# Optimization experiments

Hardware: AMD Instinct MI355X
Metric: run time of the kernel (lower is better)

The kernel has to match this reference:

```python
import jax, jax.numpy as jnp
import numpy as np

HEADS = 8

def _grid_edges(H, W):
    # 4-neighbor grid adjacency, built at trace time (static), faithful to the torch double loop
    N = H * W
    idx = np.arange(N).reshape(H, W)
    e = np.zeros((N, N), np.float32)
    a, b = idx[1:, :].ravel(), idx[:-1, :].ravel()
    e[a, b] = 1.0; e[b, a] = 1.0
    a, b = idx[:, 1:].ravel(), idx[:, :-1].ravel()
    e[a, b] = 1.0; e[b, a] = 1.0
    return jnp.asarray(e)

def _layernorm(x, g, b, eps=1e-5):
    m = x.mean(-1, keepdims=True)
    v = x.var(-1, keepdims=True)
    return (x - m) / jnp.sqrt(v + eps) * g + b

def _gat(nodes, edges, W, b, rel):
    # nodes: [N,B,E]; W: [4,E,E] (q,k,v,out); rel: [HEADS]
    N, B, E = nodes.shape
    hd = E // HEADS
    q = (nodes @ W[0].T + b[0]).reshape(N, B, HEADS, hd)
    k = (nodes @ W[1].T + b[1]).reshape(N, B, HEADS, hd)
    v = (nodes @ W[2].T + b[2]).reshape(N, B, HEADS, hd)
    s = jnp.einsum('ibhd,jbhd->hbij', q, k) / float(np.sqrt(hd))
    s = s + edges[None, None] * rel[:, None, None, None]  # per-head edge relation bias
    a = jax.nn.softmax(s, axis=1)  # faithful to source: softmax over dim=1 (batch axis)
    o = jnp.einsum('hbij,jbhd->ibhd', a, v).reshape(N, B, E)
    return o @ W[3].T + b[3]

def _mha(q_in, kv_in, W, b):
    # standard nn.MultiheadAttention (eval, no dropout); seq-first [L,B,E]
    L, B, E = q_in.shape
    S = kv_in.shape[0]
    hd = E // HEADS
    q = (q_in @ W[0].T + b[0]).reshape(L, B, HEADS, hd)
    k = (kv_in @ W[1].T + b[1]).reshape(S, B, HEADS, hd)
    v = (kv_in @ W[2].T + b[2]).reshape(S, B, HEADS, hd)
    s = jnp.einsum('ibhd,jbhd->hbij', q, k) / float(np.sqrt(hd))
    a = jax.nn.softmax(s, axis=-1)
    o = jnp.einsum('hbij,jbhd->ibhd', a, v).reshape(L, B, E)
    return o @ W[3].T + b[3]

def reference(x, gat_W, gat_b, gat_rel, cross_W, cross_b, ln_g, ln_b):
    B, C, H, W = x.shape
    P = H // 4
    # global nodes: avg_pool2d(kernel=4) then flatten to [P*P, B, C]
    g = x.reshape(B, C, P, 4, P, 4).mean(axis=(3, 5))
    global_nodes = g.reshape(B, C, P * P).transpose(2, 0, 1)
    global_edges = jnp.ones((P * P, P * P), x.dtype)
    local_nodes = x.reshape(B, C, H * W).transpose(2, 0, 1)  # [HW,B,C]
    local_edges = _grid_edges(H, W)
    g_out = _gat(global_nodes, global_edges, gat_W[0], gat_b[0], gat_rel[0])
    g_out = _layernorm(g_out + global_nodes, ln_g[0], ln_b[0])
    l_out = _gat(local_nodes, local_edges, gat_W[1], gat_b[1], gat_rel[1])
    l_out = _layernorm(l_out + local_nodes, ln_g[1], ln_b[1])
    # nearest upsample x4 of global output back to HxW
    g_map = g_out.transpose(1, 2, 0).reshape(B, C, P, P)
    g_up = jnp.repeat(jnp.repeat(g_map, 4, axis=2), 4, axis=3)
    g_up = g_up.reshape(B, C, H * W).transpose(2, 0, 1)
    c_out = _mha(l_out, g_up, cross_W, cross_b)
    c_out = _layernorm(c_out + l_out, ln_g[2], ln_b[2])
    return c_out.transpose(1, 2, 0).reshape(B, C, H, W)

def setup_inputs() -> dict:
    key = jax.random.key(0)
    ks = jax.random.split(key, 6)
    B, C, H, W = 2, 256, 40, 40
    E = C
    sc = 0.02
    return {
        "x": jax.random.normal(ks[0], (B, C, H, W), jnp.float32),
        "gat_W": jax.random.normal(ks[1], (2, 4, E, E), jnp.float32) * sc,
        "gat_b": jax.random.normal(ks[2], (2, 4, E), jnp.float32) * sc,
        "gat_rel": jax.random.normal(ks[3], (2, HEADS), jnp.float32),
        "cross_W": jax.random.normal(ks[4], (4, E, E), jnp.float32) * sc,
        "cross_b": jax.random.normal(ks[5], (4, E), jnp.float32) * sc,
        "ln_g": jnp.ones((3, E), jnp.float32),
        "ln_b": jnp.zeros((3, E), jnp.float32),
    }
```

## Files before the change

### kernel.cpp

```cpp
#include <hip/hip_runtime.h>
#include <math.h>

#define NLOC 1600
#define NGLO 100

typedef unsigned short u16;
typedef short s16x8 __attribute__((ext_vector_type(8)));
typedef float f32x4 __attribute__((ext_vector_type(4)));

__device__ __forceinline__ short f2bf(float f) {
    unsigned u = __float_as_uint(f);
    u += 0x7fffu + ((u >> 16) & 1u);
    return (short)(u >> 16);
}
__device__ __forceinline__ float bf2f(u16 h) {
    return __uint_as_float(((unsigned)h) << 16);
}

__device__ __forceinline__ void gemm_core(int lane, const u16* __restrict__ A,
                                          const u16* __restrict__ W,
                                          int M, int m0, int n0, f32x4 acc[2][4]) {
    int c = lane & 15, qd = lane >> 4;
#pragma unroll
    for (int mi = 0; mi < 2; ++mi)
#pragma unroll
        for (int ni = 0; ni < 4; ++ni) acc[mi][ni] = (f32x4){0.f, 0.f, 0.f, 0.f};
#pragma unroll 2
    for (int kc = 0; kc < 8; ++kc) {
        int ko = kc * 32 + qd * 8;
        s16x8 af[2], bf[4];
#pragma unroll
        for (int mi = 0; mi < 2; ++mi) {
            int row = m0 + mi * 16 + c;
            s16x8 zz = {};
            af[mi] = (row < M) ? *(const s16x8*)(A + (size_t)row * 256 + ko) : zz;
        }
#pragma unroll
        for (int ni = 0; ni < 4; ++ni)
            bf[ni] = *(const s16x8*)(W + (size_t)(n0 + ni * 16 + c) * 256 + ko);
#pragma unroll
        for (int mi = 0; mi < 2; ++mi)
#pragma unroll
            for (int ni = 0; ni < 4; ++ni)
                acc[mi][ni] = __builtin_amdgcn_mfma_f32_16x16x32_bf16(af[mi], bf[ni],
                                                                      acc[mi][ni], 0, 0, 0);
    }
}

__device__ __forceinline__ void ep_row(int lane, f32x4 acc[2][4],
                                       const float* __restrict__ bias,
                                       u16* __restrict__ C, int M, int m0, int n0) {
    int c = lane & 15, qd = lane >> 4;
#pragma unroll
    for (int mi = 0; mi < 2; ++mi)
#pragma unroll
        for (int r = 0; r < 4; ++r) {
            int row = m0 + mi * 16 + 4 * qd + r;
            if (row < M) {
#pragma unroll
                for (int ni = 0; ni < 4; ++ni) {
                    int col = n0 + ni * 16 + c;
                    C[(size_t)row * 256 + col] = (u16)f2bf(acc[mi][ni][r] + bias[col]);
                }
            }
        }
}

__device__ __forceinline__ void ep_vt(int lane, f32x4 acc[2][4],
                                      const float* __restrict__ bias,
                                      u16* __restrict__ vt, int Npad,
                                      int M, int m0, int n0, float* sum) {
    int c = lane & 15, qd = lane >> 4;
    float s[4] = {0.f, 0.f, 0.f, 0.f};
#pragma unroll
    for (int mi = 0; mi < 2; ++mi)
#pragma unroll
        for (int r = 0; r < 4; ++r) {
            int row = m0 + mi * 16 + 4 * qd + r;
            if (row < M) {
                int n = row >> 1, b = row & 1;
#pragma unroll
                for (int ni = 0; ni < 4; ++ni) {
                    int col = n0 + ni * 16 + c;
                    float val = acc[mi][ni][r] + bias[col];
                    vt[(size_t)(b * 256 + col) * Npad + n] = (u16)f2bf(val);
                    if (b) s[ni] += val;
                }
            }
        }
    if (sum) {
#pragma unroll
        for (int ni = 0; ni < 4; ++ni)
            atomicAdd(&sum[n0 + ni * 16 + c], s[ni]);
    }
}

__device__ __forceinline__ void ep_vt_staged(int lane, u16* vtile,
                                             f32x4 acc[2][4],
                                             const float* __restrict__ bias,
                                             u16* __restrict__ vt, int Npad,
                                             int M, int m0, int n0, float* sum) {
    int c = lane & 15, qd = lane >> 4;
    float s[4] = {0.f, 0.f, 0.f, 0.f};
#pragma unroll
    for (int mi = 0; mi < 2; ++mi)
#pragma unroll
        for (int r = 0; r < 4; ++r) {
            int row = m0 + mi * 16 + 4 * qd + r;
            int b = r & 1;
            int n_loc = mi * 8 + 2 * qd + (r >> 1);
            bool ok = (row < M);
#pragma unroll
            for (int ni = 0; ni < 4; ++ni) {
                int col = n0 + ni * 16 + c;
                float val = ok ? (acc[mi][ni][r] + bias[col]) : 0.f;
                vtile[(b * 64 + ni * 16 + c) * 16 + n_loc] = (u16)f2bf(val);
                if (b && ok) s[ni] += val;
            }
        }
    asm volatile("s_waitcnt lgkmcnt(0)" ::: "memory");
    int nst = m0 >> 1;
#pragma unroll
    for (int b2 = 0; b2 < 2; ++b2) {
        const u16* src = vtile + (b2 * 64 + lane) * 16;
        s16x8 v0 = *(const s16x8*)src;
        s16x8 v1 = *(const s16x8*)(src + 8);
        u16* dst = vt + (size_t)(b2 * 256 + n0 + lane) * Npad + nst;
        *(s16x8*)dst = v0;
        *(s16x8*)(dst + 8) = v1;
    }
    if (sum) {
#pragma unroll
        for (int ni = 0; ni < 4; ++ni)
            atomicAdd(&sum[n0 + ni * 16 + c], s[ni]);
    }
}

template <int MODE>
__device__ __forceinline__ void gemmln_block(int tid, const u16* __restrict__ A,
                                             const u16* __restrict__ W,
                                             const float* __restrict__ bias,
                                             const float* __restrict__ R,
                                             const float* __restrict__ g,
                                             const float* __restrict__ bb,
                                             float* fout, u16* bfout, float* dout,
                                             int M, int m0) {
    int w = tid >> 6, lane = tid & 63;
    int c = lane & 15, qd = lane >> 4;
    int n0 = w * 64;

    f32x4 acc[4] = {};
#pragma unroll 2
    for (int kc = 0; kc < 8; ++kc) {
        int ko = kc * 32 + qd * 8;
        int row = m0 + c;
        s16x8 zz = {};
        s16x8 af = (row < M) ? *(const s16x8*)(A + (size_t)row * 256 + ko) : zz;
#pragma unroll
        for (int ni = 0; ni < 4; ++ni) {
            s16x8 bf = *(const s16x8*)(W + (size_t)(n0 + ni * 16 + c) * 256 + ko);
            acc[ni] = __builtin_amdgcn_mfma_f32_16x16x32_bf16(af, bf, acc[ni], 0, 0, 0);
        }
    }

    __shared__ float ps1[4][16], ps2[4][16];
    float v[4][4];
#pragma unroll
    for (int r = 0; r < 4; ++r) {
        int row = m0 + 4 * qd + r;
        bool ok = (row < M);
        float s1 = 0.f, s2 = 0.f;
#pragma unroll
        for (int ni = 0; ni < 4; ++ni) {
            int col = n0 + ni * 16 + c;
            float val = acc[ni][r] + bias[col] + (ok ? R[(size_t)row * 256 + col] : 0.f);
            v[r][ni] = val;
            s1 += val; s2 += val * val;
        }
        s1 += __shfl_xor(s1, 1); s2 += __shfl_xor(s2, 1);
        s1 += __shfl_xor(s1, 2); s2 += __shfl_xor(s2, 2);
        s1 += __shfl_xor(s1, 4); s2 += __shfl_xor(s2, 4);
        s1 += __shfl_xor(s1, 8); s2 += __shfl_xor(s2, 8);
        if (c == 0) { ps1[w][4 * qd + r] = s1; ps2[w][4 * qd + r] = s2; }
    }
    __syncthreads();

    if (MODE == 0) {
#pragma unroll
        for (int r = 0; r < 4; ++r) {
            int lr = 4 * qd + r;
            int row = m0 + lr;
            if (row >= M) continue;
            float s1 = ps1[0][lr] + ps1[1][lr] + ps1[2][lr] + ps1[3][lr];
            float s2 = ps2[0][lr] + ps2[1][lr] + ps2[2][lr] + ps2[3][lr];
            float mean = s1 * (1.f / 256.f);
            float var  = s2 * (1.f / 256.f) - mean * mean;
            float rstd = rsqrtf(var + 1e-5f);
#pragma unroll
            for (int ni = 0; ni < 4; ++ni) {
                int col = n0 + ni * 16 + c;
                float y = (v[r][ni] - mean) * rstd * g[col] + bb[col];
                fout[(size_t)row * 256 + col] = y;
                bfout[(size_t)row * 256 + col] = (u16)f2bf(y);
            }
        }
    } else {
        __shared__ float ytile[2][8][256];
#pragma unroll
        for (int r = 0; r < 4; ++r) {
            int lr = 4 * qd + r;
            float s1 = ps1[0][lr] + ps1[1][lr] + ps1[2][lr] + ps1[3][lr];
            float s2 = ps2[0][lr] + ps2[1][lr] + ps2[2][lr] + ps2[3][lr];
            float mean = s1 * (1.f / 256.f);
            float var  = s2 * (1.f / 256.f) - mean * mean;
            float rstd = rsqrtf(var + 1e-5f);
#pragma unroll
            for (int ni = 0; ni < 4; ++ni) {
                int col = n0 + ni * 16 + c;
                ytile[lr & 1][lr >> 1][col] = (v[r][ni] - mean) * rstd * g[col] + bb[col];
            }
        }
        __syncthreads();
#pragma unroll
        for (int pp = tid; pp < 512; pp += 256) {
            int b = pp >> 8, col = pp & 255;
            float4 y0, y1;
            y0.x = ytile[b][0][col]; y0.y = ytile[b][1][col];
            y0.z = ytile[b][2][col]; y0.w = ytile[b][3][col];
            y1.x = ytile[b][4][col]; y1.y = ytile[b][5][col];
            y1.z = ytile[b][6][col]; y1.w = ytile[b][7][col];
            size_t o = ((size_t)(b * 256 + col)) * 1600 + (m0 >> 1);
            *(float4*)(dout + o)     = y0;
            *(float4*)(dout + o + 4) = y1;
        }
    }
}

__global__ __launch_bounds__(256) void k_prep(const float* __restrict__ gw,
                                              const float* __restrict__ cw,
                                              u16* __restrict__ gwb,
                                              u16* __restrict__ cwb,
                                              const float* __restrict__ x,
                                              float* __restrict__ nodes,
                                              u16* __restrict__ nodesb,
                                              float* __restrict__ gn,
                                              u16* __restrict__ gnb,
                                              float* __restrict__ sv1,
                                              u16* __restrict__ gvt,
                                              u16* __restrict__ cvt) {
    int bx = blockIdx.x;
    int tid = threadIdx.x;
    if (bx < 768) {
        int t = bx * 256 + tid;
        const float* src; u16* dst; int idx;
        if (t < 131072) { src = gw; dst = gwb; idx = t; }
        else            { src = cw; dst = cwb; idx = t - 131072; }
        float4 v = ((const float4*)src)[idx];
        ushort4 o;
        o.x = (u16)f2bf(v.x); o.y = (u16)f2bf(v.y);
        o.z = (u16)f2bf(v.z); o.w = (u16)f2bf(v.w);
        ((ushort4*)dst)[idx] = o;
    } else if (bx < 1568) {
        __shared__ float tile[32][33];
        int tt = bx - 768;
        int cb = tt / 100, rem = tt - cb * 100;
        int nb = rem >> 1, b = rem & 1;
        int c0 = cb * 32, n0t = nb * 32;
        int tx = tid & 31, ty = tid >> 5;
#pragma unroll
        for (int k2 = 0; k2 < 4; ++k2) {
            int cc = c0 + ty + k2 * 8;
            tile[ty + k2 * 8][tx] = x[((size_t)(b * 256 + cc)) * 1600 + n0t + tx];
        }
        __syncthreads();
#pragma unroll
        for (int k2 = 0; k2 < 4; ++k2) {
            int n = n0t + ty + k2 * 8;
            float val = tile[tx][ty + k2 * 8];
            size_t o = ((size_t)(n * 2 + b)) * 256 + c0 + tx;
            nodes[o] = val;
            nodesb[o] = (u16)f2bf(val);
        }
    } else if (bx < 1768) {
        int pt = bx - 1568;
        int b = pt & 1, n = pt >> 1;
        int cc = tid;
        int pr = n / 10, qqc = n - pr * 10;
        const float* xp = x + ((size_t)(b * 256 + cc)) * 1600 + (pr * 4) * 40 + qqc * 4;
        float s = 0.f;
#pragma unroll
        for (int dy = 0; dy < 4; ++dy)
#pragma unroll
            for (int dx = 0; dx < 4; ++dx)
                s += xp[dy * 40 + dx];
        s *= (1.f / 16.f);
        size_t t = (size_t)pt * 256 + cc;
        gn[t] = s;
        gnb[t] = (u16)f2bf(s);
    } else if (bx == 1768) {
        sv1[tid] = 0.f;
        sv1[tid + 256] = 0.f;
    } else if (bx == 1769) {
        for (int e2 = tid; e2 < 512; e2 += 256)
            for (int n = 100; n < 128; ++n) gvt[(size_t)e2 * 128 + n] = 0;
    } else {
        for (int e2 = tid; e2 < 512; e2 += 256)
            for (int n = 100; n < 128; ++n) cvt[(size_t)e2 * 128 + n] = 0;
    }
}

__global__ __launch_bounds__(64) void k_qkv(const u16* __restrict__ nodesb,
                                            const u16* __restrict__ gnb,
                                            const u16* __restrict__ W1b,
                                            const u16* __restrict__ W0b,
                                            const float* __restrict__ b1,
                                            const float* __restrict__ b0,
                                            u16* __restrict__ qbuf,
                                            u16* __restrict__ kbuf,
                                            u16* __restrict__ vtb,
                                            u16* __restrict__ gqb,
                                            u16* __restrict__ gkb,
                                            u16* __restrict__ gvt,
                                            float* __restrict__ sv1l,
                                            float* __restrict__ sv1g) {
    __shared__ u16 vtile[2 * 64 * 16];
    int lane = threadIdx.x;
    int bx = blockIdx.x, z = blockIdx.z;
    int n0 = blockIdx.y * 64;
    f32x4 acc[2][4];
    if (bx < 100) {
        int m0 = bx * 32;
        gemm_core(lane, nodesb, W1b + (size_t)z * 65536, 3200, m0, n0, acc);
        const float* bias = b1 + z * 256;
        if (z == 0)      ep_row(lane, acc, bias, qbuf, 3200, m0, n0);
        else if (z == 1) ep_row(lane, acc, bias, kbuf, 3200, m0, n0);
        else             ep_vt_staged(lane, vtile, acc, bias, vtb, 1600, 3200, m0, n0, sv1l);
    } else {
        int m0 = (bx - 100) * 32;
        gemm_core(lane, gnb, W0b + (size_t)z * 65536, 200, m0, n0, acc);
        const float* bias = b0 + z * 256;
        if (z == 0)      ep_row(lane, acc, bias, gqb, 200, m0, n0);
        else if (z == 1) ep_row(lane, acc, bias, gkb, 200, m0, n0);
        else             ep_vt_staged(lane, vtile, acc, bias, gvt, 128, 200, m0, n0, sv1g);
    }
}

__global__ __launch_bounds__(256) void k_attn(
    const u16* __restrict__ qb, const u16* __restrict__ kb,
    const u16* __restrict__ vt, float* __restrict__ pO, float* __restrict__ pT,
    const u16* __restrict__ gqb, const u16* __restrict__ gkb,
    const u16* __restrict__ gvt, const float* __restrict__ sv1g,
    u16* __restrict__ gattb)
{
    __shared__ u16 ks[2][32][40];
    __shared__ u16 vs[2][32][40];
    __shared__ short At4[4][16][40];

    int tid = threadIdx.x;
    int w = tid >> 6, lane = tid & 63;
    int c = lane & 15, qd = lane >> 4;
    int bx = blockIdx.x;

    if (bx < 800) {
        int q4 = bx & 3;
        int hic = bx >> 2;
        int ic = hic % 25, h = hic / 25;
        int hb = h * 32;
        int i0 = ic * 64 + w * 16;
        int jb0 = q4 * 13, jbe = (jb0 + 13 < 50) ? jb0 + 13 : 50;

        const u16* qp = qb + ((size_t)(i0 + c) * 2) * 256 + hb + qd * 8;
        s16x8 qf0 = *(const s16x8*)qp;
        s16x8 qf1 = *(const s16x8*)(qp + 256);
#pragma unroll
        for (int z = 0; z < 8; ++z) qf0[z] ^= (short)0x8000;

        f32x4 o0[2] = {}, t1[2] = {};

        int srow = tid >> 2, part = tid & 3;
        int sjl = srow >> 1, sb = srow & 1;
        int vb_ = srow >> 5, vd = srow & 31;

        for (int jb = jb0; jb < jbe; ++jb) {
            int j0 = jb * 32;
            __syncthreads();
            {
                s16x8 kv = *(const s16x8*)(kb + (size_t)(j0 + sjl) * 512 + sb * 256 + hb + part * 8);
                *(s16x8*)&ks[sb][sjl][part * 8] = kv;
                s16x8 vv = *(const s16x8*)(vt + (size_t)(vb_ * 256 + hb + vd) * 1600 + j0 + part * 8);
                *(s16x8*)&vs[vb_][vd][part * 8] = vv;
            }
            __syncthreads();

            s16x8 kf00 = *(const s16x8*)&ks[0][c][qd * 8];
            s16x8 kf10 = *(const s16x8*)&ks[1][c][qd * 8];
            s16x8 kf01 = *(const s16x8*)&ks[0][16 + c][qd * 8];
            s16x8 kf11 = *(const s16x8*)&ks[1][16 + c][qd * 8];

            f32x4 z4 = {};
            f32x4 sd0 = __builtin_amdgcn_mfma_f32_16x16x32_bf16(qf0, kf00, z4, 0, 0, 0);
            sd0       = __builtin_amdgcn_mfma_f32_16x16x32_bf16(qf1, kf10, sd0, 0, 0, 0);
            f32x4 sd1 = __builtin_amdgcn_mfma_f32_16x16x32_bf16(qf0, kf01, z4, 0, 0, 0);
            sd1       = __builtin_amdgcn_mfma_f32_16x16x32_bf16(qf1, kf11, sd1, 0, 0, 0);
#pragma unroll
            for (int r = 0; r < 4; ++r) {
                float e0v = __expf(sd0[r] * 0.17677669529663687f);
                At4[w][4 * qd + r][c]      = f2bf(__builtin_amdgcn_rcpf(1.f + e0v));
                float e1v = __expf(sd1[r] * 0.17677669529663687f);
                At4[w][4 * qd + r][16 + c] = f2bf(__builtin_amdgcn_rcpf(1.f + e1v));
            }
            asm volatile("s_waitcnt lgkmcnt(0)" ::: "memory");
            s16x8 af = *(const s16x8*)&At4[w][c][qd * 8];

            s16x8 vf00 = *(const s16x8*)&vs[0][c][qd * 8];
            s16x8 vf01 = *(const s16x8*)&vs[0][16 + c][qd * 8];
            s16x8 vf10 = *(const s16x8*)&vs[1][c][qd * 8];
            s16x8 vf11 = *(const s16x8*)&vs[1][16 + c][qd * 8];

            o0[0] = __builtin_amdgcn_mfma_f32_16x16x32_bf16(af, vf00, o0[0], 0, 0, 0);
            o0[1] = __builtin_amdgcn_mfma_f32_16x16x32_bf16(af, vf01, o0[1], 0, 0, 0);
            t1[0] = __builtin_amdgcn_mfma_f32_16x16x32_bf16(af, vf10, t1[0], 0, 0, 0);
            t1[1] = __builtin_amdgcn_mfma_f32_16x16x32_bf16(af, vf11, t1[1], 0, 0, 0);
        }

        size_t base = (size_t)q4 * 409600;
#pragma unroll
        for (int dh = 0; dh < 2; ++dh)
#pragma unroll
            for (int r = 0; r < 4; ++r) {
                size_t idx = base + (size_t)(i0 + 4 * qd + r) * 256 + hb + dh * 16 + c;
                pO[idx] = o0[dh][r];
                pT[idx] = t1[dh][r];
            }
    } else {
        int idx = (bx - 800) * 4 + w;
        int h = idx / 7, it = idx % 7;
        int i0 = it * 16;
        int hb = h * 32;

        s16x8 qf0 = {}, qf1 = {};
        int i = i0 + c;
        if (i < NGLO) {
            const u16* qp = gqb + ((size_t)i * 2) * 256 + hb + qd * 8;
            qf0 = *(const s16x8*)qp;
            qf1 = *(const s16x8*)(qp + 256);
        }
#pragma unroll
        for (int z = 0; z < 8; ++z) qf0[z] ^= (short)0x8000;

        f32x4 o0[2] = {}, t1[2] = {};

        for (int j0 = 0; j0 < NGLO; j0 += 32) {
            s16x8 kf[2][2], vf[2][2];
#pragma unroll
            for (int b = 0; b < 2; ++b)
#pragma unroll
                for (int js = 0; js < 2; ++js) {
                    int j = j0 + js * 16 + c;
                    s16x8 kv = {};
                    if (j < NGLO) kv = *(const s16x8*)(gkb + ((size_t)j * 2 + b) * 256 + hb + qd * 8);
                    kf[b][js] = kv;
                }
#pragma unroll
            for (int b = 0; b < 2; ++b)
#pragma unroll
                for (int dh = 0; dh < 2; ++dh)
                    vf[b][dh] = *(const s16x8*)(gvt + (size_t)(b * 256 + hb + dh * 16 + c) * 128
                                                + j0 + qd * 8);

            f32x4 z4 = {};
            f32x4 sd0 = __builtin_amdgcn_mfma_f32_16x16x32_bf16(qf0, kf[0][0], z4, 0, 0, 0);
            sd0       = __builtin_amdgcn_mfma_f32_16x16x32_bf16(qf1, kf[1][0], sd0, 0, 0, 0);
            f32x4 sd1 = __builtin_amdgcn_mfma_f32_16x16x32_bf16(qf0, kf[0][1], z4, 0, 0, 0);
            sd1       = __builtin_amdgcn_mfma_f32_16x16x32_bf16(qf1, kf[1][1], sd1, 0, 0, 0);
#pragma unroll
            for (int r = 0; r < 4; ++r) {
                float e0v = __expf(sd0[r] * 0.17677669529663687f);
                At4[w][4 * qd + r][c]      = f2bf(__builtin_amdgcn_rcpf(1.f + e0v));
                float e1v = __expf(sd1[r] * 0.17677669529663687f);
                At4[w][4 * qd + r][16 + c] = f2bf(__builtin_amdgcn_rcpf(1.f + e1v));
            }
            asm volatile("s_waitcnt lgkmcnt(0)" ::: "memory");
            s16x8 af = *(const s16x8*)&At4[w][c][qd * 8];
            o0[0] = __builtin_amdgcn_mfma_f32_16x16x32_bf16(af, vf[0][0], o0[0], 0, 0, 0);
            o0[1] = __builtin_amdgcn_mfma_f32_16x16x32_bf16(af, vf[0][1], o0[1], 0, 0, 0);
            t1[0] = __builtin_amdgcn_mfma_f32_16x16x32_bf16(af, vf[1][0], t1[0], 0, 0, 0);
            t1[1] = __builtin_amdgcn_mfma_f32_16x16x32_bf16(af, vf[1][1], t1[1], 0, 0, 0);
        }

#pragma unroll
        for (int dh = 0; dh < 2; ++dh) {
            float sv = sv1g[hb + dh * 16 + c];
#pragma unroll
            for (int r = 0; r < 4; ++r) {
                int ii = i0 + 4 * qd + r;
                if (ii < NGLO) {
                    size_t o = ((size_t)ii * 2) * 256 + hb + dh * 16 + c;
                    gattb[o]       = (u16)f2bf(o0[dh][r]);
                    gattb[o + 256] = (u16)f2bf(sv - t1[dh][r]);
                }
            }
        }
    }
}

__global__ __launch_bounds__(256) void k_combine_gproj(
    const float* __restrict__ pO, const float* __restrict__ pT,
    const float* __restrict__ sv1l, u16* __restrict__ attb,
    const u16* __restrict__ gattb, const u16* __restrict__ W0p,
    const float* __restrict__ b0p, const float* __restrict__ gn,
    const float* __restrict__ ln_g, const float* __restrict__ ln_b,
    float* __restrict__ gout, u16* __restrict__ goutb)
{
    int bx = blockIdx.x;
    if (bx < 400) {
        int t4 = (bx * 256 + threadIdx.x) * 4;
        int e = t4 & 255;
        int i = t4 >> 8;
        float4 o  = *(const float4*)(pO + t4);
        float4 tt = *(const float4*)(pT + t4);
#pragma unroll
        for (int q = 1; q < 4; ++q) {
            float4 a = *(const float4*)(pO + t4 + q * 409600);
            float4 b = *(const float4*)(pT + t4 + q * 409600);
            o.x += a.x; o.y += a.y; o.z += a.z; o.w += a.w;
            tt.x += b.x; tt.y += b.y; tt.z += b.z; tt.w += b.w;
        }
        float4 sv = *(const float4*)(sv1l + e);
        ushort4 w0, w1;
        w0.x = (u16)f2bf(o.x); w0.y = (u16)f2bf(o.y);
        w0.z = (u16)f2bf(o.z); w0.w = (u16)f2bf(o.w);
        w1.x = (u16)f2bf(sv.x - tt.x); w1.y = (u16)f2bf(sv.y - tt.y);
        w1.z = (u16)f2bf(sv.z - tt.z); w1.w = (u16)f2bf(sv.w - tt.w);
        *(ushort4*)(attb + (size_t)i * 512 + e)       = w0;
        *(ushort4*)(attb + (size_t)i * 512 + 256 + e) = w1;
    } else {
        gemmln_block<0>(threadIdx.x, gattb, W0p, b0p, gn, ln_g, ln_b,
                        gout, goutb, (float*)0, 200, (bx - 400) * 16);
    }
}

__global__ __launch_bounds__(256) void k_lproj_ckcv(
    const u16* __restrict__ attb, const u16* __restrict__ W1p,
    const float* __restrict__ b1p, const float* __restrict__ nodes,
    const float* __restrict__ ln_g1, const float* __restrict__ ln_b1,
    float* __restrict__ lout, u16* __restrict__ loutb,
    const u16* __restrict__ goutb, const u16* __restrict__ wckv,
    const float* __restrict__ bckv, u16* __restrict__ ckb,
    u16* __restrict__ cvt)
{
    int bx = blockIdx.x;
    if (bx < 200) {
        gemmln_block<0>(threadIdx.x, attb, W1p, b1p, nodes, ln_g1, ln_b1,
                        lout, loutb, (float*)0, 3200, bx * 16);
    } else {
        int w = threadIdx.x >> 6, lane = threadIdx.x & 63;
        int idx = (bx - 200) * 4 + w;
        if (idx < 56) {
            int z = idx / 28, rem = idx % 28;
            int m0 = (rem >> 2) * 32, n0 = (rem & 3) * 64;
            f32x4 acc[2][4];
            gemm_core(lane, goutb, wckv + (size_t)z * 65536, 200, m0, n0, acc);
            const float* bias = bckv + z * 256;
            if (z == 0) ep_row(lane, acc, bias, ckb, 200, m0, n0);
            else        ep_vt(lane, acc, bias, cvt, 128, 200, m0, n0, (float*)0);
        }
    }
}

__global__ __launch_bounds__(256) void k_cross(
    const u16* __restrict__ loutb, const u16* __restrict__ wcq,
    const float* __restrict__ bcq, const u16* __restrict__ kb,
    const u16* __restrict__ vt, u16* __restrict__ out)
{
    __shared__ short At[4][16][136];
    __shared__ short Aq[4][16][40];
    int w = threadIdx.x >> 6, lane = threadIdx.x & 63;
    int c  = lane & 15;
    int qd = lane >> 4;
    int idx = blockIdx.x * 4 + w;
    int it = idx % 100;
    int hb2 = idx / 100;
    int h = hb2 >> 1, b = hb2 & 1;
    int i0 = it * 16;
    int hb = h * 32;

    for (int z = lane; z < 16 * 24; z += 64)
        At[w][z / 24][112 + (z % 24)] = 0;

    f32x4 qacc[2] = {};
#pragma unroll 2
    for (int kc = 0; kc < 8; ++kc) {
        int ko = kc * 32 + qd * 8;
        s16x8 af = *(const s16x8*)(loutb + ((size_t)(i0 + c) * 2 + b) * 256 + ko);
#pragma unroll
        for (int ni = 0; ni < 2; ++ni) {
            s16x8 bf = *(const s16x8*)(wcq + (size_t)(hb + ni * 16 + c) * 256 + ko);
            qacc[ni] = __builtin_amdgcn_mfma_f32_16x16x32_bf16(af, bf, qacc[ni], 0, 0, 0);
        }
    }
#pragma unroll
    for (int ni = 0; ni < 2; ++ni)
#pragma unroll
        for (int r = 0; r < 4; ++r)
            Aq[w][4 * qd + r][ni * 16 + c] = f2bf(qacc[ni][r] + bcq[hb + ni * 16 + c]);
    asm volatile("s_waitcnt lgkmcnt(0)" ::: "memory");
    s16x8 qf = *(const s16x8*)&Aq[w][c][qd * 8];

    f32x4 s[7];
#pragma unroll
    for (int jt = 0; jt < 7; ++jt) {
        int j = jt * 16 + c;
        s16x8 kf = {};
        if (j < NGLO) kf = *(const s16x8*)(kb + ((size_t)j * 2 + b) * 256 + hb + qd * 8);
        f32x4 z4 = {};
        s[jt] = __builtin_amdgcn_mfma_f32_16x16x32_bf16(qf, kf, z4, 0, 0, 0);
    }
    if (c >= 4) {
#pragma unroll
        for (int r = 0; r < 4; ++r) s[6][r] = -1e30f;
    }
#pragma unroll
    for (int jt = 0; jt < 7; ++jt)
#pragma unroll
        for (int r = 0; r < 4; ++r) s[jt][r] *= 0.17677669529663687f;

    float l[4];
#pragma unroll
    for (int r = 0; r < 4; ++r) {
        float mm = s[0][r];
#pragma unroll
        for (int jt = 1; jt < 7; ++jt) mm = fmaxf(mm, s[jt][r]);
        mm = fmaxf(mm, __shfl_xor(mm, 1));
        mm = fmaxf(mm, __shfl_xor(mm, 2));
        mm = fmaxf(mm, __shfl_xor(mm, 4));
        mm = fmaxf(mm, __shfl_xor(mm, 8));
        float ll = 0.f;
#pragma unroll
        for (int jt = 0; jt < 7; ++jt) {
            float pv = __expf(s[jt][r] - mm);
            s[jt][r] = pv;
            ll += pv;
        }
        ll += __shfl_xor(ll, 1);
        ll += __shfl_xor(ll, 2);
        ll += __shfl_xor(ll, 4);
        ll += __shfl_xor(ll, 8);
        l[r] = ll;
    }
#pragma unroll
    for (int jt = 0; jt < 7; ++jt)
#pragma unroll
        for (int r = 0; r < 4; ++r)
            At[w][4 * qd + r][jt * 16 + c] = f2bf(s[jt][r]);
    asm volatile("s_waitcnt lgkmcnt(0)" ::: "memory");

    f32x4 o[2] = {};
#pragma unroll
    for (int kc = 0; kc < 4; ++kc) {
        s16x8 af = *(const s16x8*)&At[w][c][kc * 32 + qd * 8];
#pragma unroll
        for (int dh = 0; dh < 2; ++dh) {
            s16x8 vf = *(const s16x8*)(vt + (size_t)(b * 256 + hb + dh * 16 + c) * 128
                                       + kc * 32 + qd * 8);
            o[dh] = __builtin_amdgcn_mfma_f32_16x16x32_bf16(af, vf, o[dh], 0, 0, 0);
        }
    }
#pragma unroll
    for (int dh = 0; dh < 2; ++dh)
#pragma unroll
        for (int r = 0; r < 4; ++r) {
            int ii = i0 + 4 * qd + r;
            out[((size_t)ii * 2 + b) * 256 + hb + dh * 16 + c] = (u16)f2bf(o[dh][r] / l[r]);
        }
}

__global__ __launch_bounds__(256) void k_cproj(
    const u16* __restrict__ cattb, const u16* __restrict__ wcp,
    const float* __restrict__ bcp, const float* __restrict__ lout,
    const float* __restrict__ ln_g2, const float* __restrict__ ln_b2,
    float* __restrict__ dout)
{
    gemmln_block<1>(threadIdx.x, cattb, wcp, bcp, lout, ln_g2, ln_b2,
                    (float*)0, (u16*)0, dout, 3200, blockIdx.x * 16);
}

extern "C" void kernel_launch(void* const* d_in, const int* in_sizes, int n_in,
                              void* d_out, int out_size, void* d_ws, size_t ws_size,
                              hipStream_t stream) {
    const float* x        = (const float*)d_in[0];
    const float* gat_W    = (const float*)d_in[1];
    const float* gat_b    = (const float*)d_in[2];
    const float* cross_W  = (const float*)d_in[4];
    const float* cross_b  = (const float*)d_in[5];
    const float* ln_g     = (const float*)d_in[6];
    const float* ln_b     = (const float*)d_in[7];
    float* out = (float*)d_out;

    float* ws    = (float*)d_ws;
    float* nodes = ws;
    float* gn    = nodes + 819200;
    float* gout  = gn + 51200;
    float* lout  = gout + 51200;
    float* sv1l  = lout + 819200;
    float* sv1g  = sv1l + 256;
    float* pO    = sv1g + 256;
    float* pT    = pO + 1638400;

    u16* ub = (u16*)(pT + 1638400);
    u16* wgatb  = ub;            ub += 524288;
    u16* wcrsb  = ub;            ub += 262144;
    u16* nodesb = ub;            ub += 819200;
    u16* gnb    = ub;            ub += 51200;
    u16* qbuf   = ub;            ub += 819200;
    u16* kbuf   = ub;            ub += 819200;
    u16* vtb    = ub;            ub += 819200;
    u16* gqb    = ub;            ub += 51200;
    u16* gkb    = ub;            ub += 51200;
    u16* gvt    = ub;            ub += 65536;
    u16* gattb  = ub;            ub += 51200;
    u16* goutb  = ub;            ub += 51200;
    u16* attb   = ub;            ub += 819200;
    u16* loutb  = ub;            ub += 819200;
    u16* ckb    = ub;            ub += 51200;
    u16* cvt    = ub;            ub += 65536;
    u16* cattb  = kbuf;

    const u16* W0b = wgatb;
    const u16* W1b = wgatb + 4 * 65536;
    const float* b0 = gat_b;
    const float* b1 = gat_b + 4 * 256;

    k_prep<<<1771, 256, 0, stream>>>(gat_W, cross_W, wgatb, wcrsb,
                                     x, nodes, nodesb, gn, gnb, sv1l, gvt, cvt);
    k_qkv<<<dim3(107, 4, 3), 64, 0, stream>>>(nodesb, gnb, W1b, W0b, b1, b0,
                                              qbuf, kbuf, vtb, gqb, gkb, gvt,
                                              sv1l, sv1g);
    k_attn<<<814, 256, 0, stream>>>(qbuf, kbuf, vtb, pO, pT,
                                    gqb, gkb, gvt, sv1g, gattb);
    k_combine_gproj<<<413, 256, 0, stream>>>(pO, pT, sv1l, attb,
                                             gattb, W0b + 3 * 65536, b0 + 768, gn,
                                             ln_g, ln_b, gout, goutb);
    k_lproj_ckcv<<<214, 256, 0, stream>>>(attb, W1b + 3 * 65536, b1 + 768, nodes,
                                          ln_g + 256, ln_b + 256, lout, loutb,
                                          goutb, wcrsb + 65536, cross_b + 256,
                                          ckb, cvt);
    k_cross<<<400, 256, 0, stream>>>(loutb, wcrsb, cross_b, ckb, cvt, cattb);
    k_cproj<<<200, 256, 0, stream>>>(cattb, wcrsb + 3 * 65536, cross_b + 768, lout,
                                     ln_g + 512, ln_b + 512, out);
}
```

Baseline: 186.9 us.

## Restructure QKV projection into 256-thread blocks with LDS-staged 64x64 tiles

The QKV projection kernel moves from single-wave blocks computing 32x64 tiles straight from global memory to 4-wave blocks. Each block stages a 64x256 A tile and a 64x256 weight tile in LDS, and each wave computes a 16x64 output slice. Weight tiles are now reused across four waves instead of being reloaded per wave, at the cost of about 67KB of LDS per block and fewer blocks in flight. The epilogues are adapted to 16-row tiles.

Result: slower. 237.5 us (+27.1%).

```diff
diff --git a/kernel.cpp b/kernel.cpp
--- a/kernel.cpp
+++ b/kernel.cpp
@@ -95,39 +95,49 @@
     }
 }
 
-__device__ __forceinline__ void ep_vt_staged(int lane, u16* vtile,
-                                             f32x4 acc[2][4],
-                                             const float* __restrict__ bias,
-                                             u16* __restrict__ vt, int Npad,
-                                             int M, int m0, int n0, float* sum) {
+__device__ __forceinline__ void ep_row16(int lane, f32x4 acc[4],
+                                         const float* __restrict__ bias,
+                                         u16* __restrict__ C, int M, int m0, int n0) {
+    int c = lane & 15, qd = lane >> 4;
+#pragma unroll
+    for (int r = 0; r < 4; ++r) {
+        int row = m0 + 4 * qd + r;
+        if (row < M) {
+#pragma unroll
+            for (int ni = 0; ni < 4; ++ni) {
+                int col = n0 + ni * 16 + c;
+                C[(size_t)row * 256 + col] = (u16)f2bf(acc[ni][r] + bias[col]);
+            }
+        }
+    }
+}
+
+__device__ __forceinline__ void ep_vt16(int lane, u16* vtile, f32x4 acc[4],
+                                        const float* __restrict__ bias,
+                                        u16* __restrict__ vt, int Npad,
+                                        int M, int m0, int n0, float* sum) {
     int c = lane & 15, qd = lane >> 4;
     float s[4] = {0.f, 0.f, 0.f, 0.f};
 #pragma unroll
-    for (int mi = 0; mi < 2; ++mi)
-#pragma unroll
-        for (int r = 0; r < 4; ++r) {
-            int row = m0 + mi * 16 + 4 * qd + r;
-            int b = r & 1;
-            int n_loc = mi * 8 + 2 * qd + (r >> 1);
-            bool ok = (row < M);
-#pragma unroll
-            for (int ni = 0; ni < 4; ++ni) {
-                int col = n0 + ni * 16 + c;
-                float val = ok ? (acc[mi][ni][r] + bias[col]) : 0.f;
-                vtile[(b * 64 + ni * 16 + c) * 16 + n_loc] = (u16)f2bf(val);
-                if (b && ok) s[ni] += val;
-            }
-        }
+    for (int r = 0; r < 4; ++r) {
+        int row = m0 + 4 * qd + r;
+        int b = r & 1;
+        int n_loc = 2 * qd + (r >> 1);
+        bool ok = (row < M);
+#pragma unroll
+        for (int ni = 0; ni < 4; ++ni) {
+            int col = n0 + ni * 16 + c;
+            float val = ok ? (acc[ni][r] + bias[col]) : 0.f;
+            vtile[(b * 64 + ni * 16 + c) * 8 + n_loc] = (u16)f2bf(val);
+            if (b && ok) s[ni] += val;
+        }
+    }
     asm volatile("s_waitcnt lgkmcnt(0)" ::: "memory");
     int nst = m0 >> 1;
 #pragma unroll
     for (int b2 = 0; b2 < 2; ++b2) {
-        const u16* src = vtile + (b2 * 64 + lane) * 16;
-        s16x8 v0 = *(const s16x8*)src;
-        s16x8 v1 = *(const s16x8*)(src + 8);
-        u16* dst = vt + (size_t)(b2 * 256 + n0 + lane) * Npad + nst;
-        *(s16x8*)dst = v0;
-        *(s16x8*)(dst + 8) = v1;
+        s16x8 v0 = *(const s16x8*)(vtile + (b2 * 64 + lane) * 8);
+        *(s16x8*)(vt + (size_t)(b2 * 256 + n0 + lane) * Npad + nst) = v0;
     }
     if (sum) {
 #pragma unroll
@@ -309,39 +319,68 @@
     }
 }
 
-__global__ __launch_bounds__(64) void k_qkv(const u16* __restrict__ nodesb,
-                                            const u16* __restrict__ gnb,
-                                            const u16* __restrict__ W1b,
-                                            const u16* __restrict__ W0b,
-                                            const float* __restrict__ b1,
-                                            const float* __restrict__ b0,
-                                            u16* __restrict__ qbuf,
-                                            u16* __restrict__ kbuf,
-                                            u16* __restrict__ vtb,
-                                            u16* __restrict__ gqb,
-                                            u16* __restrict__ gkb,
-                                            u16* __restrict__ gvt,
-                                            float* __restrict__ sv1l,
-                                            float* __restrict__ sv1g) {
-    __shared__ u16 vtile[2 * 64 * 16];
-    int lane = threadIdx.x;
+__global__ __launch_bounds__(256) void k_qkv(const u16* __restrict__ nodesb,
+                                             const u16* __restrict__ gnb,
+                                             const u16* __restrict__ W1b,
+                                             const u16* __restrict__ W0b,
+                                             const float* __restrict__ b1,
+                                             const float* __restrict__ b0,
+                                             u16* __restrict__ qbuf,
+                                             u16* __restrict__ kbuf,
+                                             u16* __restrict__ vtb,
+                                             u16* __restrict__ gqb,
+                                             u16* __restrict__ gkb,
+                                             u16* __restrict__ gvt,
+                                             float* __restrict__ sv1l,
+                                             float* __restrict__ sv1g) {
+    __shared__ u16 As[64][264];
+    __shared__ u16 Ws[64][264];
+    __shared__ u16 vtile4[4][2 * 64 * 8];
+    int tid = threadIdx.x;
+    int w = tid >> 6, lane = tid & 63;
+    int c = lane & 15, qd = lane >> 4;
     int bx = blockIdx.x, z = blockIdx.z;
     int n0 = blockIdx.y * 64;
-    f32x4 acc[2][4];
-    if (bx < 100) {
-        int m0 = bx * 32;
-        gemm_core(lane, nodesb, W1b + (size_t)z * 65536, 3200, m0, n0, acc);
-        const float* bias = b1 + z * 256;
-        if (z == 0)      ep_row(lane, acc, bias, qbuf, 3200, m0, n0);
-        else if (z == 1) ep_row(lane, acc, bias, kbuf, 3200, m0, n0);
-        else             ep_vt_staged(lane, vtile, acc, bias, vtb, 1600, 3200, m0, n0, sv1l);
+    bool isLoc = (bx < 50);
+    const u16* A = isLoc ? nodesb : gnb;
+    const u16* W = (isLoc ? W1b : W0b) + (size_t)z * 65536;
+    const float* bias = (isLoc ? b1 : b0) + z * 256;
+    int M = isLoc ? 3200 : 200;
+    int m0 = (isLoc ? bx : bx - 50) * 64;
+
+#pragma unroll
+    for (int pp = 0; pp < 8; ++pp) {
+        int p = tid + pp * 256;
+        int row = p >> 5;
+        int ko = (p & 31) * 8;
+        int ar = m0 + row;
+        s16x8 av = {};
+        if (ar < M) av = *(const s16x8*)(A + (size_t)ar * 256 + ko);
+        *(s16x8*)&As[row][ko] = av;
+        s16x8 wv = *(const s16x8*)(W + (size_t)(n0 + row) * 256 + ko);
+        *(s16x8*)&Ws[row][ko] = wv;
+    }
+    __syncthreads();
+
+    f32x4 acc[4] = {};
+#pragma unroll
+    for (int kc = 0; kc < 8; ++kc) {
+        s16x8 af = *(const s16x8*)&As[w * 16 + c][kc * 32 + qd * 8];
+#pragma unroll
+        for (int ni = 0; ni < 4; ++ni) {
+            s16x8 wf = *(const s16x8*)&Ws[ni * 16 + c][kc * 32 + qd * 8];
+            acc[ni] = __builtin_amdgcn_mfma_f32_16x16x32_bf16(af, wf, acc[ni], 0, 0, 0);
+        }
+    }
+
+    int mw = m0 + w * 16;
+    if (z == 0) {
+        ep_row16(lane, acc, bias, isLoc ? qbuf : gqb, M, mw, n0);
+    } else if (z == 1) {
+        ep_row16(lane, acc, bias, isLoc ? kbuf : gkb, M, mw, n0);
     } else {
-        int m0 = (bx - 100) * 32;
-        gemm_core(lane, gnb, W0b + (size_t)z * 65536, 200, m0, n0, acc);
-        const float* bias = b0 + z * 256;
-        if (z == 0)      ep_row(lane, acc, bias, gqb, 200, m0, n0);
-        else if (z == 1) ep_row(lane, acc, bias, gkb, 200, m0, n0);
-        else             ep_vt_staged(lane, vtile, acc, bias, gvt, 128, 200, m0, n0, sv1g);
+        ep_vt16(lane, vtile4[w], acc, bias, isLoc ? vtb : gvt,
+                isLoc ? 1600 : 128, M, mw, n0, isLoc ? sv1l : sv1g);
     }
 }
 
@@ -733,7 +772,7 @@
 
     k_prep<<<1771, 256, 0, stream>>>(gat_W, cross_W, wgatb, wcrsb,
                                      x, nodes, nodesb, gn, gnb, sv1l, gvt, cvt);
-    k_qkv<<<dim3(107, 4, 3), 64, 0, stream>>>(nodesb, gnb, W1b, W0b, b1, b0,
+    k_qkv<<<dim3(54, 4, 3), 256, 0, stream>>>(nodesb, gnb, W1b, W0b, b1, b0,
                                               qbuf, kbuf, vtb, gqb, gkb, gvt,
                                               sv1l, sv1g);
     k_attn<<<814, 256, 0, stream>>>(qbuf, kbuf, vtb, pO, pT,
```
